# Kernel tuning notes

Hardware: AMD Instinct MI355X
Metric: run time of the kernel (lower is better)

Reference implementation:

```python
import jax, jax.numpy as jnp
import numpy as np

B, S, D, H = 2, 2048, 2048, 16
HD = D // H
ALIBI_BIAS_MAX = 8
NEG_INF = -1e9  # used only via float('-inf') literal below


def build_attn_mask(n_heads, seq_len, alibi_bias_max=8, dtype=jnp.float32):
    # causal mask: -inf strictly above diagonal
    causal = jnp.triu(jnp.full((seq_len, seq_len), -jnp.inf, dtype=dtype), k=1)
    # full alibi bias: -|i-j| scaled per head by 1/2**(m_h)
    rel = jnp.arange(1 - seq_len, 1, dtype=dtype)  # [S]
    bias = rel[None, :] - rel[:, None]             # [S,S]
    bias = -jnp.abs(bias)
    m = jnp.arange(1, n_heads + 1, dtype=dtype) * (alibi_bias_max / n_heads)
    slopes = 1.0 / (2.0 ** m)                      # [H]
    a_bias = bias[None, :, :] * slopes[:, None, None]  # [H,S,S]
    return causal[None, :, :] + a_bias


def setup_inputs() -> dict:
    key = jax.random.key(0)
    ks = jax.random.split(key, 6)
    x = jax.random.normal(ks[0], (B, S, D), dtype=jnp.float32)
    key_padding_mask = jnp.ones((B, S), dtype=bool)  # True = keep (module inverts before torch)
    attn_mask = build_attn_mask(H, S, ALIBI_BIAS_MAX)
    scale = 1.0 / np.sqrt(D)
    in_proj_w = jax.random.normal(ks[1], (3 * D, D), dtype=jnp.float32) * scale
    in_proj_b = jax.random.normal(ks[2], (3 * D,), dtype=jnp.float32) * 0.01
    out_w = jax.random.normal(ks[3], (D, D), dtype=jnp.float32) * scale
    out_b = jax.random.normal(ks[4], (D,), dtype=jnp.float32) * 0.01
    return {"x": x, "key_padding_mask": key_padding_mask, "attn_mask": attn_mask,
            "in_proj_w": in_proj_w, "in_proj_b": in_proj_b,
            "out_w": out_w, "out_b": out_b}


def reference(x, key_padding_mask, attn_mask, in_proj_w, in_proj_b, out_w, out_b):
    # fused QKV projection (torch MultiheadAttention in_proj)
    qkv = jnp.einsum('bsd,ed->bse', x, in_proj_w) + in_proj_b  # [B,S,3D]
    q, k, v = jnp.split(qkv, 3, axis=-1)
    # [B,H,S,hd]
    q = q.reshape(B, S, H, HD).transpose(0, 2, 1, 3)
    k = k.reshape(B, S, H, HD).transpose(0, 2, 1, 3)
    v = v.reshape(B, S, H, HD).transpose(0, 2, 1, 3)
    scores = jnp.einsum('bhqd,bhkd->bhqk', q, k) / jnp.sqrt(jnp.float32(HD))
    scores = scores + attn_mask[None]  # causal + alibi, [1,H,S,S]
    # key_padding_mask True = keep; masked keys -> -inf
    scores = jnp.where(key_padding_mask[:, None, None, :], scores, -jnp.inf)
    attn = jax.nn.softmax(scores, axis=-1)  # [B,H,S,S]
    ctx = jnp.einsum('bhqk,bhkd->bhqd', attn, v)
    ctx = ctx.transpose(0, 2, 1, 3).reshape(B, S, D)
    out = jnp.einsum('bsd,ed->bse', ctx, out_w) + out_b
    # need_weights=True, average_attn_weights default True -> mean over heads
    avg_attn = attn.mean(axis=1)  # [B,S,S]
    return out, avg_attn
```

## Files before the change

### kernel.cpp

```cpp
#include <hip/hip_runtime.h>
#include <math.h>

#define BB 2
#define SS 2048
#define DD 2048
#define HH 16
#define HDIM 128
#define QKVP 6144
#define NEG_INIT  -1.0e30f
#define NEG_CLAMP -3.0e4f

typedef __attribute__((ext_vector_type(8))) short s8v;
typedef __attribute__((ext_vector_type(4))) float f4v;

typedef const unsigned __attribute__((address_space(1)))* gas_ptr;
typedef unsigned __attribute__((address_space(3)))* las_ptr;

__device__ __forceinline__ void gld16(const short* g, short* l) {
  __builtin_amdgcn_global_load_lds((gas_ptr)g, (las_ptr)l, 16, 0, 0);
}

__device__ __forceinline__ short f2bf(float f) {
  unsigned u = __float_as_uint(f);
  unsigned r = (u + 0x7FFFu + ((u >> 16) & 1u)) >> 16;
  return (short)(unsigned short)r;
}

__global__ void conv_bf16(const float* __restrict__ src, short* __restrict__ dst,
                          int n8) {
  int t = blockIdx.x * blockDim.x + threadIdx.x;
  if (t >= n8) return;
  const float* s = src + (size_t)t * 8;
  s8v o;
#pragma unroll
  for (int i = 0; i < 8; i++) o[i] = f2bf(s[i]);
  ((s8v*)dst)[t] = o;
}

template <typename TOUT>
__global__ __launch_bounds__(256) void gemm_bt_bias(
    const short* __restrict__ A, const short* __restrict__ Bm,
    const float* __restrict__ bias, TOUT* __restrict__ C,
    int M, int N, int K)
{
  __shared__ short As[2][128 * 64];
  __shared__ short Bs[2][128 * 64];
  const int tid = threadIdx.x;
  const int lane = tid & 63, wid = tid >> 6;
  const int wm = wid >> 1, wn = wid & 1;
  const int ln = lane & 15, quad = lane >> 4;
  const int m0 = blockIdx.y * 128, n0 = blockIdx.x * 128;

  f4v acc[4][4];
#pragma unroll
  for (int i = 0; i < 4; i++)
#pragma unroll
    for (int j = 0; j < 4; j++) acc[i][j] = {0.f, 0.f, 0.f, 0.f};

  const int srow = (lane >> 3);
  const int scol = (((lane & 7) ^ srow)) * 8;
  const short* a_g = A  + (size_t)(m0 + wid * 32 + srow) * K + scol;
  const short* b_g = Bm + (size_t)(n0 + wid * 32 + srow) * K + scol;

#pragma unroll
  for (int i = 0; i < 4; i++) {
    gld16(a_g + (size_t)i * 8 * K, &As[0][(wid * 32 + i * 8) * 64]);
    gld16(b_g + (size_t)i * 8 * K, &Bs[0][(wid * 32 + i * 8) * 64]);
  }
  __syncthreads();

  int cur = 0;
  for (int kt = 0; kt < K; kt += 64) {
    if (kt + 64 < K) {
      const short* an = a_g + kt + 64;
      const short* bn = b_g + kt + 64;
#pragma unroll
      for (int i = 0; i < 4; i++) {
        gld16(an + (size_t)i * 8 * K, &As[cur ^ 1][(wid * 32 + i * 8) * 64]);
        gld16(bn + (size_t)i * 8 * K, &Bs[cur ^ 1][(wid * 32 + i * 8) * 64]);
      }
    }
#pragma unroll
    for (int kc = 0; kc < 2; kc++) {
      s8v af[4], bfr[4];
#pragma unroll
      for (int i = 0; i < 4; i++) {
        int row = wm * 64 + i * 16 + ln;
        int c16 = (kc * 4 + quad) ^ (ln & 7);
        af[i] = *(const s8v*)&As[cur][row * 64 + c16 * 8];
      }
#pragma unroll
      for (int j = 0; j < 4; j++) {
        int row = wn * 64 + j * 16 + ln;
        int c16 = (kc * 4 + quad) ^ (ln & 7);
        bfr[j] = *(const s8v*)&Bs[cur][row * 64 + c16 * 8];
      }
#pragma unroll
      for (int i = 0; i < 4; i++)
#pragma unroll
        for (int j = 0; j < 4; j++)
          acc[i][j] = __builtin_amdgcn_mfma_f32_16x16x32_bf16(af[i], bfr[j], acc[i][j], 0, 0, 0);
    }
    __syncthreads();
    cur ^= 1;
  }
#pragma unroll
  for (int j = 0; j < 4; j++) {
    int col = n0 + wn * 64 + j * 16 + ln;
    float bv = bias[col];
#pragma unroll
    for (int i = 0; i < 4; i++) {
      int rbase = m0 + wm * 64 + i * 16 + quad * 4;
#pragma unroll
      for (int r = 0; r < 4; r++) {
        float val = acc[i][j][r] + bv;
        if constexpr (sizeof(TOUT) == 4)
          C[(size_t)(rbase + r) * N + col] = val;
        else
          C[(size_t)(rbase + r) * N + col] = f2bf(val);
      }
    }
  }
}

__global__ __launch_bounds__(256) void transpose_v(const short* __restrict__ qkv,
                                                   short* __restrict__ vT) {
  __shared__ short tile[64 * 72];
  const int bh = blockIdx.z;
  const int b = bh >> 4;
  const int hsel = bh & 15;
  const int s0 = blockIdx.x * 64;
  const int hd0 = blockIdx.y * 64;
  const int t = threadIdx.x;
  const int r = t >> 3, c8 = t & 7;
#pragma unroll
  for (int half = 0; half < 2; half++) {
    int rr = r + half * 32;
    s8v v = *(const s8v*)&qkv[(size_t)(b * SS + s0 + rr) * QKVP + 4096 + hsel * HDIM + hd0 + c8 * 8];
    *(s8v*)&tile[rr * 72 + c8 * 8] = v;
  }
  __syncthreads();
#pragma unroll
  for (int half = 0; half < 2; half++) {
    int rr = r + half * 32;
    s8v o;
#pragma unroll
    for (int j = 0; j < 8; j++) o[j] = tile[(c8 * 8 + j) * 72 + rr];
    *(s8v*)&vT[((size_t)bh * HDIM + hd0 + rr) * SS + s0 + c8 * 8] = o;
  }
}

__global__ __launch_bounds__(512, 4) void flash_fwd(
    const short* __restrict__ qkv, const short* __restrict__ vT,
    float* __restrict__ lse, short* __restrict__ ctx)
{
  __shared__ short Ks[64 * 136];
  __shared__ short Vs[128 * 72];
  __shared__ short plds[8][16 * 72];

  const int g = blockIdx.x;
  const int b = g >> 8;
  const int h = (g >> 4) & 15;
  const int qh = g & 15;
  const int qt = b ? qh : 15 - qh;

  const int bh = b * HH + h;
  const int tid = threadIdx.x, lane = tid & 63, wid = tid >> 6;
  const int ln = lane & 15, quad = lane >> 4;
  const int q0 = qt * 128 + wid * 16;

  const short* qb = qkv + (size_t)b * SS * QKVP + h * HDIM;
  const short* kb = qb + 2048;
  const short* vb = vT + (size_t)bh * HDIM * SS;

  const int krow = tid >> 3, kc0 = (tid & 7) * 8;
  const int vrow = tid >> 2, vc0 = (tid & 3) * 8;
  const short* kgp = kb + (size_t)krow * QKVP + kc0;
  const short* vgp = vb + (size_t)vrow * SS + vc0;
  short* kls = &Ks[krow * 136 + kc0];
  short* vls = &Vs[vrow * 72 + vc0];

  const float slope = exp2f(-0.5f * (float)(h + 1));
  const float scale = 0.08838834764831845f;

  s8v aq[4];
#pragma unroll
  for (int kc = 0; kc < 4; kc++)
    aq[kc] = *(const s8v*)&qb[(size_t)(q0 + ln) * QKVP + kc * 32 + quad * 8];

  s8v k0r = ((const s8v*)kgp)[0], k1r = *(const s8v*)(kgp + 64);
  s8v v0r = ((const s8v*)vgp)[0], v1r = *(const s8v*)(vgp + 32);

  f4v o[8];
#pragma unroll
  for (int d = 0; d < 8; d++) o[d] = {0.f, 0.f, 0.f, 0.f};
  float mrow[4], lrow[4];
#pragma unroll
  for (int r = 0; r < 4; r++) { mrow[r] = NEG_INIT; lrow[r] = 0.0f; }

  const int nkt = 2 * qt + 2;
  for (int kt = 0; kt < nkt; kt++) {
    __syncthreads();
    *(s8v*)kls = k0r;  *(s8v*)(kls + 64) = k1r;
    *(s8v*)vls = v0r;  *(s8v*)(vls + 32) = v1r;
    if (kt < nkt - 1) {
      const short* kn = kgp + (size_t)(kt + 1) * 64 * QKVP;
      const short* vn = vgp + (kt + 1) * 64;
      k0r = ((const s8v*)kn)[0]; k1r = *(const s8v*)(kn + 64);
      v0r = ((const s8v*)vn)[0]; v1r = *(const s8v*)(vn + 32);
    }
    __syncthreads();

    if (kt * 64 > q0 + 15) continue;

    f4v sacc[4];
    __builtin_amdgcn_s_setprio(1);
#pragma unroll
    for (int ks = 0; ks < 4; ks++) {
      f4v z = {0.f, 0.f, 0.f, 0.f};
      if (kt * 64 + ks * 16 <= q0 + 15) {
#pragma unroll
        for (int kc = 0; kc < 4; kc++) {
          s8v bk = *(const s8v*)&Ks[(ks * 16 + ln) * 136 + kc * 32 + quad * 8];
          z = __builtin_amdgcn_mfma_f32_16x16x32_bf16(aq[kc], bk, z, 0, 0, 0);
        }
      }
      sacc[ks] = z;
    }
    __builtin_amdgcn_s_setprio(0);
    float sv[4][4];
#pragma unroll
    for (int ks = 0; ks < 4; ks++)
#pragma unroll
      for (int r = 0; r < 4; r++) {
        int i = q0 + quad * 4 + r;
        int j = kt * 64 + ks * 16 + ln;
        int di = i - j;
        sv[ks][r] = (di >= 0) ? fmaf(sacc[ks][r], scale, -(float)di * slope)
                              : NEG_CLAMP;
      }
    float mx4[4];
#pragma unroll
    for (int r = 0; r < 4; r++) {
      float mx = fmaxf(fmaxf(sv[0][r], sv[1][r]), fmaxf(sv[2][r], sv[3][r]));
#pragma unroll
      for (int off = 1; off < 16; off <<= 1)
        mx = fmaxf(mx, __shfl_xor(mx, off, 64));
      mx4[r] = mx;
    }
    const bool resc = __any((mx4[0] > mrow[0] + 8.0f) || (mx4[1] > mrow[1] + 8.0f) ||
                            (mx4[2] > mrow[2] + 8.0f) || (mx4[3] > mrow[3] + 8.0f));
    float al[4] = {1.0f, 1.0f, 1.0f, 1.0f};
    if (resc) {
#pragma unroll
      for (int r = 0; r < 4; r++) {
        float mnew = fmaxf(mrow[r], mx4[r]);
        al[r] = __expf(mrow[r] - mnew);
        mrow[r] = mnew;
      }
    }
    float ps[4] = {0.f, 0.f, 0.f, 0.f};
    short pb[4][4];
#pragma unroll
    for (int ks = 0; ks < 4; ks++)
#pragma unroll
      for (int r = 0; r < 4; r++) {
        float p = __expf(sv[ks][r] - mrow[r]);
        ps[r] += p;
        pb[ks][r] = f2bf(p);
      }
#pragma unroll
    for (int r = 0; r < 4; r++) {
      float s = ps[r];
#pragma unroll
      for (int off = 1; off < 16; off <<= 1) s += __shfl_xor(s, off, 64);
      lrow[r] = lrow[r] * al[r] + s;
    }
    if (resc) {
#pragma unroll
      for (int d = 0; d < 8; d++)
#pragma unroll
        for (int r = 0; r < 4; r++) o[d][r] *= al[r];
    }
#pragma unroll
    for (int ks = 0; ks < 4; ks++)
#pragma unroll
      for (int r = 0; r < 4; r++)
        plds[wid][(quad * 4 + r) * 72 + ks * 16 + ln] = pb[ks][r];
    __builtin_amdgcn_s_setprio(1);
#pragma unroll
    for (int kc2 = 0; kc2 < 2; kc2++) {
      s8v ap = *(const s8v*)&plds[wid][ln * 72 + kc2 * 32 + quad * 8];
#pragma unroll
      for (int d = 0; d < 8; d++) {
        s8v bv = *(const s8v*)&Vs[(d * 16 + ln) * 72 + kc2 * 32 + quad * 8];
        o[d] = __builtin_amdgcn_mfma_f32_16x16x32_bf16(ap, bv, o[d], 0, 0, 0);
      }
    }
    __builtin_amdgcn_s_setprio(0);
  }
  float inv[4];
#pragma unroll
  for (int r = 0; r < 4; r++) inv[r] = 1.0f / lrow[r];
#pragma unroll
  for (int d = 0; d < 8; d++)
#pragma unroll
    for (int r = 0; r < 4; r++) {
      int qrow = q0 + quad * 4 + r;
      ctx[((size_t)(b * SS + qrow)) * DD + h * HDIM + d * 16 + ln] = f2bf(o[d][r] * inv[r]);
    }
#pragma unroll
  for (int r = 0; r < 4; r++)
    if (ln == r)
      lse[(size_t)bh * SS + q0 + quad * 4 + r] = mrow[r] + __logf(lrow[r]);
}

__global__ __launch_bounds__(256, 4) void avg_attn_kernel(
    const short* __restrict__ qkv, const float* __restrict__ lse,
    float* __restrict__ avg)
{
  __shared__ short Ks[64 * 136];
  const int ktile = blockIdx.x, qtile = blockIdx.y, b = blockIdx.z;
  const int tid = threadIdx.x, lane = tid & 63, wid = tid >> 6;
  const int ln = lane & 15, quad = lane >> 4;
  const int q0 = qtile * 64 + wid * 16;
  const int k0 = ktile * 64;
  float acc[4][4];
#pragma unroll
  for (int ks = 0; ks < 4; ks++)
#pragma unroll
    for (int r = 0; r < 4; r++) acc[ks][r] = 0.0f;

  if (ktile <= qtile) {
    const float scale = 0.08838834764831845f;
    const int krow = tid >> 2, kch = (tid & 3) * 8;
    const short* kg0 = qkv + (size_t)(b * SS + k0 + krow) * QKVP + 2048 + kch;
    short* kls = &Ks[krow * 136 + kch];
    s8v kreg[4];
#pragma unroll
    for (int j = 0; j < 4; j++) kreg[j] = *(const s8v*)(kg0 + j * 32);
    for (int hh = 0; hh < HH; hh++) {
      __syncthreads();
#pragma unroll
      for (int j = 0; j < 4; j++) *(s8v*)(kls + j * 32) = kreg[j];
      if (hh < HH - 1) {
        const short* kn = kg0 + (hh + 1) * HDIM;
#pragma unroll
        for (int j = 0; j < 4; j++) kreg[j] = *(const s8v*)(kn + j * 32);
      }
      __syncthreads();
      const int bh = b * HH + hh;
      const float slope = exp2f(-0.5f * (float)(hh + 1));
      const short* qb = qkv + (size_t)b * SS * QKVP + hh * HDIM;
      s8v aq[4];
#pragma unroll
      for (int kc = 0; kc < 4; kc++)
        aq[kc] = *(const s8v*)&qb[(size_t)(q0 + ln) * QKVP + kc * 32 + quad * 8];
      float lsev[4];
#pragma unroll
      for (int r = 0; r < 4; r++) lsev[r] = lse[(size_t)bh * SS + q0 + quad * 4 + r];
#pragma unroll
      for (int ks = 0; ks < 4; ks++) {
        if (k0 + ks * 16 > q0 + 15) continue;
        f4v z = {0.f, 0.f, 0.f, 0.f};
#pragma unroll
        for (int kc = 0; kc < 4; kc++) {
          s8v bk = *(const s8v*)&Ks[(ks * 16 + ln) * 136 + kc * 32 + quad * 8];
          z = __builtin_amdgcn_mfma_f32_16x16x32_bf16(aq[kc], bk, z, 0, 0, 0);
        }
#pragma unroll
        for (int r = 0; r < 4; r++) {
          int i = q0 + quad * 4 + r;
          int j = k0 + ks * 16 + ln;
          int di = i - j;
          float svv = (di >= 0) ? fmaf(z[r], scale, -(float)di * slope) : NEG_CLAMP;
          acc[ks][r] += __expf(svv - lsev[r]);
        }
      }
    }
  }
  const float inv16 = 1.0f / 16.0f;
#pragma unroll
  for (int ks = 0; ks < 4; ks++)
#pragma unroll
    for (int r = 0; r < 4; r++)
      avg[((size_t)b * SS + q0 + quad * 4 + r) * SS + k0 + ks * 16 + ln] =
          acc[ks][r] * inv16;
}

extern "C" void kernel_launch(void* const* d_in, const int* in_sizes, int n_in,
                              void* d_out, int out_size, void* d_ws, size_t ws_size,
                              hipStream_t stream)
{
  const float *x = nullptr, *w_in = nullptr, *b_in = nullptr,
              *w_out = nullptr, *b_out = nullptr;
  for (int idx = 0; idx < n_in; idx++) {
    switch (in_sizes[idx]) {
      case 8388608:  x     = (const float*)d_in[idx]; break;
      case 12582912: w_in  = (const float*)d_in[idx]; break;
      case 6144:     b_in  = (const float*)d_in[idx]; break;
      case 4194304:  w_out = (const float*)d_in[idx]; break;
      case 2048:     b_out = (const float*)d_in[idx]; break;
      default: break;
    }
  }

  char* ws = (char*)d_ws;
  short* qkv = (short*)(ws);
  short* xb  = (short*)(ws + 50331648);
  short* vT  = (short*)(ws + 50331648);
  short* wib = (short*)(ws + 67108864);
  short* ctx = (short*)(ws + 67108864);
  float* lse = (float*)(ws + 83886080);
  short* wob = (short*)(ws + 92274688);

  float* outp = (float*)d_out;
  float* avgp = outp + (size_t)BB * SS * DD;

  conv_bf16<<<4096, 256, 0, stream>>>(x, xb, 1048576);
  conv_bf16<<<6144, 256, 0, stream>>>(w_in, wib, 1572864);
  conv_bf16<<<2048, 256, 0, stream>>>(w_out, wob, 524288);

  gemm_bt_bias<short><<<dim3(QKVP / 128, (BB * SS) / 128), 256, 0, stream>>>(
      xb, wib, b_in, qkv, BB * SS, QKVP, DD);
  transpose_v<<<dim3(32, 2, 32), 256, 0, stream>>>(qkv, vT);
  flash_fwd<<<dim3(512, 1, 1), 512, 0, stream>>>(qkv, vT, lse, ctx);
  avg_attn_kernel<<<dim3(32, 32, 2), 256, 0, stream>>>(qkv, lse, avgp);
  gemm_bt_bias<float><<<dim3(DD / 128, (BB * SS) / 128), 256, 0, stream>>>(
      ctx, wob, b_out, outp, BB * SS, DD, DD);
}
```

Measured before the change: 708.0 us.

## Double-buffer K tiles and prefetch Q/LSE in avg-attention kernel

Rewrites the per-head loop of the head-averaged attention-weights kernel to double-buffer the K tile in shared memory, so each head's loop needs one barrier instead of two. It also prefetches the next head's Q fragments and LSE values into registers while the current head computes. The causal mask and distance values are now computed once outside the head loop, and the alibi bias and LSE are folded into one per-element constant, so the inner exp takes a single fma. The cost is twice the LDS per block and more live registers, which can lower occupancy at launch bounds (256,4).

```diff
diff --git a/kernel.cpp b/kernel.cpp
--- a/kernel.cpp
+++ b/kernel.cpp
@@ -319,7 +319,7 @@
     const short* __restrict__ qkv, const float* __restrict__ lse,
     float* __restrict__ avg)
 {
-  __shared__ short Ks[64 * 136];
+  __shared__ short Ks[2][64 * 136];
   const int ktile = blockIdx.x, qtile = blockIdx.y, b = blockIdx.z;
   const int tid = threadIdx.x, lane = tid & 63, wid = tid >> 6;
   const int ln = lane & 15, quad = lane >> 4;
@@ -335,48 +335,87 @@
     const float scale = 0.08838834764831845f;
     const int krow = tid >> 2, kch = (tid & 3) * 8;
     const short* kg0 = qkv + (size_t)(b * SS + k0 + krow) * QKVP + 2048 + kch;
-    short* kls = &Ks[krow * 136 + kch];
+    const short* qb0 = qkv + (size_t)(b * SS + q0 + ln) * QKVP;
+    const float* lse0 = lse + (size_t)(b * HH) * SS + q0 + quad * 4;
+
+    float df[4][4];
+    bool  mk[4][4];
+#pragma unroll
+    for (int ks = 0; ks < 4; ks++)
+#pragma unroll
+      for (int r = 0; r < 4; r++) {
+        int di = (q0 + quad * 4 + r) - (k0 + ks * 16 + ln);
+        df[ks][r] = (float)di;
+        mk[ks][r] = (di >= 0);
+      }
+
     s8v kreg[4];
 #pragma unroll
     for (int j = 0; j < 4; j++) kreg[j] = *(const s8v*)(kg0 + j * 32);
+#pragma unroll
+    for (int j = 0; j < 4; j++)
+      *(s8v*)&Ks[0][krow * 136 + kch + j * 32] = kreg[j];
+#pragma unroll
+    for (int j = 0; j < 4; j++) kreg[j] = *(const s8v*)(kg0 + HDIM + j * 32);
+    s8v aqr[4];
+#pragma unroll
+    for (int kc = 0; kc < 4; kc++)
+      aqr[kc] = *(const s8v*)&qb0[kc * 32 + quad * 8];
+    float lsr[4];
+#pragma unroll
+    for (int r = 0; r < 4; r++) lsr[r] = lse0[r];
+    __syncthreads();
+
+    int cur = 0;
     for (int hh = 0; hh < HH; hh++) {
-      __syncthreads();
-#pragma unroll
-      for (int j = 0; j < 4; j++) *(s8v*)(kls + j * 32) = kreg[j];
+      s8v aq[4];
+#pragma unroll
+      for (int kc = 0; kc < 4; kc++) aq[kc] = aqr[kc];
+      float ls4[4];
+#pragma unroll
+      for (int r = 0; r < 4; r++) ls4[r] = lsr[r];
+
       if (hh < HH - 1) {
-        const short* kn = kg0 + (hh + 1) * HDIM;
-#pragma unroll
-        for (int j = 0; j < 4; j++) kreg[j] = *(const s8v*)(kn + j * 32);
-      }
-      __syncthreads();
-      const int bh = b * HH + hh;
+#pragma unroll
+        for (int j = 0; j < 4; j++)
+          *(s8v*)&Ks[cur ^ 1][krow * 136 + kch + j * 32] = kreg[j];
+        if (hh < HH - 2) {
+          const short* kn = kg0 + (hh + 2) * HDIM;
+#pragma unroll
+          for (int j = 0; j < 4; j++) kreg[j] = *(const s8v*)(kn + j * 32);
+        }
+        const short* qn = qb0 + (hh + 1) * HDIM;
+#pragma unroll
+        for (int kc = 0; kc < 4; kc++)
+          aqr[kc] = *(const s8v*)&qn[kc * 32 + quad * 8];
+        const float* ln2 = lse0 + (size_t)(hh + 1) * SS;
+#pragma unroll
+        for (int r = 0; r < 4; r++) lsr[r] = ln2[r];
+      }
+
       const float slope = exp2f(-0.5f * (float)(hh + 1));
-      const short* qb = qkv + (size_t)b * SS * QKVP + hh * HDIM;
-      s8v aq[4];
-#pragma unroll
-      for (int kc = 0; kc < 4; kc++)
-        aq[kc] = *(const s8v*)&qb[(size_t)(q0 + ln) * QKVP + kc * 32 + quad * 8];
-      float lsev[4];
-#pragma unroll
-      for (int r = 0; r < 4; r++) lsev[r] = lse[(size_t)bh * SS + q0 + quad * 4 + r];
+      float cc[4][4];
+#pragma unroll
+      for (int ks = 0; ks < 4; ks++)
+#pragma unroll
+        for (int r = 0; r < 4; r++)
+          cc[ks][r] = mk[ks][r] ? fmaf(df[ks][r], -slope, -ls4[r]) : NEG_CLAMP;
+
 #pragma unroll
       for (int ks = 0; ks < 4; ks++) {
         if (k0 + ks * 16 > q0 + 15) continue;
         f4v z = {0.f, 0.f, 0.f, 0.f};
 #pragma unroll
         for (int kc = 0; kc < 4; kc++) {
-          s8v bk = *(const s8v*)&Ks[(ks * 16 + ln) * 136 + kc * 32 + quad * 8];
+          s8v bk = *(const s8v*)&Ks[cur][(ks * 16 + ln) * 136 + kc * 32 + quad * 8];
           z = __builtin_amdgcn_mfma_f32_16x16x32_bf16(aq[kc], bk, z, 0, 0, 0);
         }
 #pragma unroll
-        for (int r = 0; r < 4; r++) {
-          int i = q0 + quad * 4 + r;
-          int j = k0 + ks * 16 + ln;
-          int di = i - j;
-          float svv = (di >= 0) ? fmaf(z[r], scale, -(float)di * slope) : NEG_CLAMP;
-          acc[ks][r] += __expf(svv - lsev[r]);
-        }
-      }
+        for (int r = 0; r < 4; r++)
+          acc[ks][r] += __expf(fmaf(z[r], scale, cc[ks][r]));
+      }
+      __syncthreads();
+      cur ^= 1;
     }
   }
   const float inv16 = 1.0f / 16.0f;
```

New measurement: 707.6 us. Within noise of the previous version (-0.1%).
